# Performance work log

Measured on AMD Instinct MI355X. Metric: run time of the kernel, lower is better.

Reference implementation:

```python
import jax, jax.numpy as jnp
import numpy as np

LN_EPS = 1e-6          # flax nn.LayerNorm default
ATTN_EPS = 1e-9        # numerical_stabilizer default


def ln_points(x, scale, bias):
    """flax LayerNorm(reduction_axes=-2): stats over points axis, affine over feature axis."""
    mu = jnp.mean(x, axis=-2, keepdims=True)
    var = jnp.mean(jnp.square(x), axis=-2, keepdims=True) - jnp.square(mu)
    return (x - mu) * jax.lax.rsqrt(var + LN_EPS) * scale + bias


def self_attention_layer(x, wq_i, bq_i, wk_i, bk_i, wv_i, bv_i, wo_i, bo_i, ls_i, lb_i):
    # 1x1 convs == pointwise linears
    q = x @ wq_i + bq_i                                  # [B,N,C]
    k = x @ wk_i + bk_i
    v = x @ wv_i + bv_i
    attn = jnp.einsum('bmc,bnc->bmn', q, k)              # [B,M,N]
    attn = jax.nn.softmax(attn, axis=-1)
    # extra offset-attention renorm: divide by column sums (axis=1)
    attn = attn / (ATTN_EPS + jnp.sum(attn, axis=1, keepdims=True))
    # einsum '...MN,...NC->...NC' reduces M: scales v by column sums
    col = jnp.sum(attn, axis=1)                          # [B,N]
    out = col[..., None] * v                             # [B,N,C]
    out = out @ wo_i + bo_i
    out = jax.nn.relu(ln_points(out, ls_i, lb_i))
    return out + x


def setup_inputs() -> dict:
    key = jax.random.key(0)
    ks = jax.random.split(key, 16)
    B, N, IN, C, F, L = 2, 4096, 3, 256, 1024, 4
    s_in = 1.0 / np.sqrt(IN)
    s_c = 1.0 / np.sqrt(C)
    s_f = 1.0 / np.sqrt(L * C)
    return {
        'inputs': jax.random.normal(ks[0], (B, N, IN), jnp.float32),
        'w0': jax.random.normal(ks[1], (IN, C), jnp.float32) * s_in,
        'b0': jnp.zeros((C,), jnp.float32),
        'ln0_s': jnp.ones((C,), jnp.float32),
        'ln0_b': jnp.zeros((C,), jnp.float32),
        'w1': jax.random.normal(ks[2], (C, C), jnp.float32) * s_c,
        'b1': jnp.zeros((C,), jnp.float32),
        'ln1_s': jnp.ones((C,), jnp.float32),
        'ln1_b': jnp.zeros((C,), jnp.float32),
        'wq': jax.random.normal(ks[3], (L, C, C), jnp.float32) * s_c,
        'bq': jnp.zeros((L, C), jnp.float32),
        'wk': jax.random.normal(ks[4], (L, C, C), jnp.float32) * s_c,
        'bk': jnp.zeros((L, C), jnp.float32),
        'wv': jax.random.normal(ks[5], (L, C, C), jnp.float32) * s_c,
        'bv': jnp.zeros((L, C), jnp.float32),
        'wo': jax.random.normal(ks[6], (L, C, C), jnp.float32) * s_c,
        'bo': jnp.zeros((L, C), jnp.float32),
        'attn_ln_s': jnp.ones((L, C), jnp.float32),
        'attn_ln_b': jnp.zeros((L, C), jnp.float32),
        'wf': jax.random.normal(ks[7], (L * C, F), jnp.float32) * s_f,
        'bf': jnp.zeros((F,), jnp.float32),
    }


def reference(inputs, w0, b0, ln0_s, ln0_b, w1, b1, ln1_s, ln1_b,
              wq, bq, wk, bk, wv, bv, wo, bo, attn_ln_s, attn_ln_b, wf, bf):
    # pre-conv stack
    out = ln_points(inputs @ w0 + b0, ln0_s, ln0_b)
    out = ln_points(out @ w1 + b1, ln1_s, ln1_b)
    # attention stack (4 structurally identical layers, concatenated)
    attn_outs = []
    for i in range(wq.shape[0]):
        out = self_attention_layer(out, wq[i], bq[i], wk[i], bk[i],
                                   wv[i], bv[i], wo[i], bo[i],
                                   attn_ln_s[i], attn_ln_b[i])
        attn_outs.append(out)
    out = jnp.concatenate(attn_outs, axis=-1)            # [B,N,4C]
    out = out @ wf + bf                                  # [B,N,F]
    return out
```

## Files before the change

### kernel.cpp

```cpp
#include <hip/hip_runtime.h>

#define BB 2
#define NN 4096
#define CC 256
#define FF 1024
#define NLAYER 4
#define RR (BB*NN)
#define SPL 16
#define QKLD (3*CC)
#define NEG_BIG (-1e30f)

typedef _Float16 h16;
typedef __attribute__((ext_vector_type(8))) _Float16 half8;
typedef __attribute__((ext_vector_type(4))) float f32x4;
typedef __attribute__((ext_vector_type(16))) float f32x16;

__device__ __forceinline__ void gload16(const h16* g, h16* l) {
    __builtin_amdgcn_global_load_lds((const __attribute__((address_space(1))) void*)g,
                                     (__attribute__((address_space(3))) void*)l, 16, 0, 0);
}

template<int ROWS>
__device__ __forceinline__ void stage_rows(const h16* __restrict__ src, int ld,
    int row0, int c0, h16* lds, int tid)
{
    int w = tid >> 6;
    #pragma unroll
    for (int t = 0; t < ROWS/32; ++t) {
        int slot = t*256 + tid;
        int row = slot >> 3;
        int pp  = slot & 7;
        int piece = pp ^ (row & 7);
        gload16(src + (size_t)(row0 + row)*ld + c0 + piece*8,
                lds + (t*256 + w*64)*8);
    }
}

__device__ __forceinline__ half8 frag_ld(const h16* lds, int row, int pl) {
    return *(const half8*)(lds + row*64 + ((pl ^ (row & 7))*8));
}

__global__ __launch_bounds__(256) void pct_wtrans(const float* __restrict__ W,
    h16* __restrict__ WT, int K, int N, int dstride)
{
    __shared__ h16 t[32][33];
    const float* Wl = W + (size_t)blockIdx.z*K*N;
    h16* WTl = WT + (size_t)blockIdx.z*dstride;
    int k0 = blockIdx.x*32, n0 = blockIdx.y*32;
    int tx = threadIdx.x & 31, ty = threadIdx.x >> 5;
    #pragma unroll
    for (int i = ty; i < 32; i += 8)
        t[i][tx] = (h16)Wl[(size_t)(k0+i)*N + n0 + tx];
    __syncthreads();
    #pragma unroll
    for (int i = ty; i < 32; i += 8)
        WTl[(size_t)(n0+i)*K + k0 + tx] = t[tx][i];
}

__global__ __launch_bounds__(256) void pct_bias3(const float* __restrict__ bq,
    const float* __restrict__ bk, const float* __restrict__ bv, float* __restrict__ o)
{
    int l = blockIdx.x, c = threadIdx.x;
    o[l*QKLD + c]        = bq[l*CC + c];
    o[l*QKLD + CC + c]   = bk[l*CC + c];
    o[l*QKLD + 2*CC + c] = bv[l*CC + c];
}

__global__ __launch_bounds__(256) void pct_embed(const float* __restrict__ inp,
    const float* __restrict__ w0, const float* __restrict__ b0, h16* __restrict__ out)
{
    int r = blockIdx.x, c = threadIdx.x;
    float a0 = inp[r*3+0], a1 = inp[r*3+1], a2 = inp[r*3+2];
    out[(size_t)r*CC + c] = (h16)(b0[c] + a0*w0[c] + a1*w0[CC+c] + a2*w0[2*CC+c]);
}

__global__ __launch_bounds__(256) void pct_colstat(const h16* __restrict__ x, int ldx,
    float* __restrict__ sums)
{
    __shared__ float red[2][8][256];
    int b = blockIdx.x, blk = blockIdx.y;
    int rt = threadIdx.x >> 5;
    int cg = (threadIdx.x & 31) * 8;
    const h16* p = x + ((size_t)b*NN + (size_t)blk*64 + rt)*ldx + cg;
    float s1[8] = {0,0,0,0,0,0,0,0}, s2[8] = {0,0,0,0,0,0,0,0};
    #pragma unroll
    for (int i = 0; i < 8; ++i) {
        half8 v = *(const half8*)(p + (size_t)i*8*ldx);
        #pragma unroll
        for (int j = 0; j < 8; ++j) { float f = (float)v[j]; s1[j] += f; s2[j] += f*f; }
    }
    #pragma unroll
    for (int j = 0; j < 8; ++j) { red[0][rt][cg+j] = s1[j]; red[1][rt][cg+j] = s2[j]; }
    __syncthreads();
    int c = threadIdx.x;
    float t1 = 0.f, t2 = 0.f;
    #pragma unroll
    for (int r = 0; r < 8; ++r) { t1 += red[0][r][c]; t2 += red[1][r][c]; }
    atomicAdd(&sums[(b*CC + c)*2 + 0], t1);
    atomicAdd(&sums[(b*CC + c)*2 + 1], t2);
}

__global__ __launch_bounds__(256) void pct_lnapply(const h16* __restrict__ x, int ldx,
    const float* __restrict__ sums, const float* __restrict__ scale, const float* __restrict__ bias,
    const h16* __restrict__ res, int ldr, h16* __restrict__ out, int ldo,
    int do_relu)
{
    int r = blockIdx.x*8 + (threadIdx.x >> 5);
    int cg = (threadIdx.x & 31) * 8;
    int b = r / NN;
    half8 xv = *(const half8*)(x + (size_t)r*ldx + cg);
    half8 rv;
    if (res) rv = *(const half8*)(res + (size_t)r*ldr + cg);
    half8 ov;
    #pragma unroll
    for (int j = 0; j < 8; ++j) {
        int c = cg + j;
        float s1 = sums[(b*CC + c)*2], s2 = sums[(b*CC + c)*2 + 1];
        float mu  = s1 * (1.f/NN);
        float var = s2 * (1.f/NN) - mu*mu;
        float rstd = rsqrtf(var + 1e-6f);
        float y = ((float)xv[j] - mu) * rstd * scale[c] + bias[c];
        if (do_relu) y = fmaxf(y, 0.f);
        if (res) y += (float)rv[j];
        ov[j] = (h16)y;
    }
    *(half8*)(out + (size_t)r*ldo + cg) = ov;
}

template<int BN, bool OUT_F32>
__global__ __launch_bounds__(256) void pct_gemm_f16(
    const h16* __restrict__ A, int lda,
    const h16* __restrict__ WT, const float* __restrict__ bias,
    void* __restrict__ outp, int ldo, int K, const float* __restrict__ rowS)
{
    constexpr int BJ = BN/2;
    constexpr int NF = BJ/16;
    __shared__ __align__(16) h16 Asm[128*64];
    __shared__ __align__(16) h16 Bsm[BN*64];
    const int tid = threadIdx.x;
    const int lane = tid & 63, w = tid >> 6;
    const int ln = lane & 15, lq = lane >> 4;
    const int wr = w >> 1, wc = w & 1;
    const int m0 = blockIdx.x*128, n0 = blockIdx.y*BN;
    f32x4 acc[4][NF];
    #pragma unroll
    for (int i = 0; i < 4; ++i)
        #pragma unroll
        for (int j = 0; j < NF; ++j) acc[i][j] = (f32x4){0.f,0.f,0.f,0.f};
    for (int k0 = 0; k0 < K; k0 += 64) {
        stage_rows<128>(A, lda, m0, k0, Asm, tid);
        stage_rows<BN>(WT, K, n0, k0, Bsm, tid);
        __syncthreads();
        #pragma unroll
        for (int kk = 0; kk < 2; ++kk) {
            half8 af[4], bfr[NF];
            #pragma unroll
            for (int i = 0; i < 4; ++i) af[i] = frag_ld(Asm, wr*64 + i*16 + ln, kk*4 + lq);
            #pragma unroll
            for (int j = 0; j < NF; ++j) bfr[j] = frag_ld(Bsm, wc*BJ + j*16 + ln, kk*4 + lq);
            #pragma unroll
            for (int i = 0; i < 4; ++i)
                #pragma unroll
                for (int j = 0; j < NF; ++j)
                    acc[i][j] = __builtin_amdgcn_mfma_f32_16x16x32_f16(af[i], bfr[j], acc[i][j], 0, 0, 0);
        }
        __syncthreads();
    }
    #pragma unroll
    for (int j = 0; j < NF; ++j) {
        int col = n0 + wc*BJ + j*16 + ln;
        float bv = bias[col];
        #pragma unroll
        for (int i = 0; i < 4; ++i) {
            #pragma unroll
            for (int r = 0; r < 4; ++r) {
                int row = m0 + wr*64 + i*16 + lq*4 + r;
                float sc = 1.f;
                if (rowS) { float s = rowS[row]; sc = s / (1e-9f + s); }
                float v = acc[i][j][r] * sc + bv;
                if (OUT_F32) ((float*)outp)[(size_t)row*ldo + col] = v;
                else ((h16*)outp)[(size_t)row*ldo + col] = (h16)v;
            }
        }
    }
}

__global__ __launch_bounds__(256) void attn_rowstats(const h16* __restrict__ QKV,
    float2* __restrict__ part)
{
    __shared__ __align__(16) h16 Ks[2][128*64];
    const int b = blockIdx.x, mt = blockIdx.y, sp = blockIdx.z;
    const int tid = threadIdx.x;
    const int lane = tid & 63, w = tid >> 6;
    const int ln2 = lane & 31, h = lane >> 5;
    const h16* qb = QKV + (size_t)b*NN*QKLD;
    const h16* kb = qb + CC;
    const int m0 = mt*128;
    const h16* qrow = qb + (size_t)(m0 + w*32 + ln2)*QKLD + h*8;
    half8 qreg[16];
    #pragma unroll
    for (int i = 0; i < 16; ++i) qreg[i] = *(const half8*)(qrow + i*16);

    const int nbeg = sp*(NN/SPL);
    const int NT = (NN/SPL)/128;
    float rm = NEG_BIG, rs = 0.f;

    stage_rows<128>(kb, QKLD, nbeg, 0, Ks[0], tid);
    int id = 0;
    for (int t = 0; t < NT; ++t) {
        f32x16 acc[4];
        #pragma unroll
        for (int j = 0; j < 4; ++j) acc[j] = (f32x16)(0.f);
        #pragma unroll
        for (int c = 0; c < 4; ++c, ++id) {
            __syncthreads();
            if (id + 1 < NT*4)
                stage_rows<128>(kb, QKLD, nbeg + ((id+1) >> 2)*128, ((id+1) & 3)*64,
                                Ks[(id+1) & 1], tid);
            const h16* buf = Ks[id & 1];
            #pragma unroll
            for (int kk = 0; kk < 4; ++kk) {
                half8 bq = qreg[c*4 + kk];
                #pragma unroll
                for (int j = 0; j < 4; ++j) {
                    half8 af = frag_ld(buf, j*32 + ln2, kk*2 + h);
                    acc[j] = __builtin_amdgcn_mfma_f32_32x32x16_f16(af, bq, acc[j], 0, 0, 0);
                }
            }
        }
        float tm = NEG_BIG;
        #pragma unroll
        for (int j = 0; j < 4; ++j)
            #pragma unroll
            for (int g = 0; g < 16; g += 2)
                tm = fmaxf(tm, fmaxf(acc[j][g], acc[j][g+1]));
        if (tm > rm) { rs *= __expf(rm - tm); rm = tm; }
        float s = 0.f;
        #pragma unroll
        for (int j = 0; j < 4; ++j)
            #pragma unroll
            for (int g = 0; g < 16; ++g)
                s += __expf(acc[j][g] - rm);
        rs += s;
    }
    float mo = __shfl_xor(rm, 32, 64);
    float so = __shfl_xor(rs, 32, 64);
    float mn = fmaxf(rm, mo);
    float sm = rs*__expf(rm - mn) + so*__expf(mo - mn);
    if (lane < 32) {
        int m = m0 + w*32 + ln2;
        part[((size_t)b*NN + m)*SPL + sp] = make_float2(mn, sm);
    }
}

__global__ __launch_bounds__(256) void pct_rowcomb(const float2* __restrict__ part,
    float2* __restrict__ rstat)
{
    int idx = blockIdx.x*256 + threadIdx.x;
    const float2* p = part + (size_t)idx*SPL;
    float m = NEG_BIG;
    #pragma unroll
    for (int s = 0; s < SPL; ++s) m = fmaxf(m, p[s].x);
    float sum = 0.f;
    #pragma unroll
    for (int s = 0; s < SPL; ++s) sum += p[s].y * __expf(p[s].x - m);
    rstat[idx] = make_float2(m, 1.0f / sum);
}

__global__ __launch_bounds__(256) void attn_colsums(const h16* __restrict__ QKV,
    const float2* __restrict__ rstat, float* __restrict__ S)
{
    __shared__ __align__(16) h16 Qs[2][128*64];
    const int b = blockIdx.x, nt = blockIdx.y, sp = blockIdx.z;
    const int tid = threadIdx.x;
    const int lane = tid & 63, w = tid >> 6;
    const int ln2 = lane & 31, h = lane >> 5;
    const h16* qb = QKV + (size_t)b*NN*QKLD;
    const h16* kb = qb + CC;
    const float2* rst = rstat + (size_t)b*NN;
    const int n0 = nt*128;
    const h16* krow = kb + (size_t)(n0 + w*32 + ln2)*QKLD + h*8;
    half8 kreg[16];
    #pragma unroll
    for (int i = 0; i < 16; ++i) kreg[i] = *(const half8*)(krow + i*16);

    const int mbeg = sp*(NN/SPL);
    const int NT = (NN/SPL)/128;
    float cs = 0.f;

    stage_rows<128>(qb, QKLD, mbeg, 0, Qs[0], tid);
    int id = 0;
    for (int t = 0; t < NT; ++t) {
        f32x16 acc[4];
        #pragma unroll
        for (int j = 0; j < 4; ++j) acc[j] = (f32x16)(0.f);
        #pragma unroll
        for (int c = 0; c < 4; ++c, ++id) {
            __syncthreads();
            if (id + 1 < NT*4)
                stage_rows<128>(qb, QKLD, mbeg + ((id+1) >> 2)*128, ((id+1) & 3)*64,
                                Qs[(id+1) & 1], tid);
            const h16* buf = Qs[id & 1];
            #pragma unroll
            for (int kk = 0; kk < 4; ++kk) {
                half8 bk = kreg[c*4 + kk];
                #pragma unroll
                for (int j = 0; j < 4; ++j) {
                    half8 af = frag_ld(buf, j*32 + ln2, kk*2 + h);
                    acc[j] = __builtin_amdgcn_mfma_f32_32x32x16_f16(af, bk, acc[j], 0, 0, 0);
                }
            }
        }
        int mt0 = mbeg + t*128;
        #pragma unroll
        for (int j = 0; j < 4; ++j) {
            #pragma unroll
            for (int g = 0; g < 16; ++g) {
                int m = mt0 + j*32 + (g & 3) + 8*(g >> 2) + 4*h;
                float2 st = rst[m];
                cs += __expf(acc[j][g] - st.x) * st.y;
            }
        }
    }
    cs += __shfl_xor(cs, 32, 64);
    if (lane < 32) {
        int n = n0 + w*32 + ln2;
        atomicAdd(&S[(size_t)b*NN + n], cs);
    }
}

extern "C" void kernel_launch(void* const* d_in, const int* in_sizes, int n_in,
                              void* d_out, int out_size, void* d_ws, size_t ws_size,
                              hipStream_t stream)
{
    const float* inp  = (const float*)d_in[0];
    const float* w0   = (const float*)d_in[1];
    const float* b0   = (const float*)d_in[2];
    const float* ln0s = (const float*)d_in[3];
    const float* ln0b = (const float*)d_in[4];
    const float* w1   = (const float*)d_in[5];
    const float* b1   = (const float*)d_in[6];
    const float* ln1s = (const float*)d_in[7];
    const float* ln1b = (const float*)d_in[8];
    const float* wq   = (const float*)d_in[9];
    const float* bq   = (const float*)d_in[10];
    const float* wk   = (const float*)d_in[11];
    const float* bk   = (const float*)d_in[12];
    const float* wv   = (const float*)d_in[13];
    const float* bv   = (const float*)d_in[14];
    const float* wo   = (const float*)d_in[15];
    const float* bo   = (const float*)d_in[16];
    const float* alns = (const float*)d_in[17];
    const float* alnb = (const float*)d_in[18];
    const float* wf   = (const float*)d_in[19];
    const float* bfb  = (const float*)d_in[20];
    float* out = (float*)d_out;

    char* p = (char*)d_ws;
    auto alloc = [&](size_t bytes) { char* r = p; p += (bytes + 255) & ~255ULL; return r; };
    h16* t0    = (h16*)alloc((size_t)RR*CC*2);
    h16* t1    = (h16*)alloc((size_t)RR*CC*2);
    h16* t2    = (h16*)alloc((size_t)RR*CC*2);
    h16* x1    = (h16*)alloc((size_t)RR*CC*2);
    h16* qkv   = (h16*)alloc((size_t)RR*QKLD*2);
    h16* oh    = (h16*)alloc((size_t)RR*CC*2);
    h16* xcat  = (h16*)alloc((size_t)RR*FF*2);
    h16* w1T   = (h16*)alloc((size_t)CC*CC*2);
    h16* wqkvT = (h16*)alloc((size_t)NLAYER*QKLD*CC*2);
    h16* woT   = (h16*)alloc((size_t)NLAYER*CC*CC*2);
    h16* wfT   = (h16*)alloc((size_t)FF*FF*2);
    float* bqkv  = (float*)alloc((size_t)NLAYER*QKLD*4);
    float2* part  = (float2*)alloc((size_t)RR*SPL*8);
    float2* rstat = (float2*)alloc((size_t)RR*8);
    float* Ssum  = (float*)alloc((size_t)NLAYER*RR*4);
    float* lns   = (float*)alloc((size_t)6*BB*CC*2*4);

    dim3 blk(256);

    hipMemsetAsync(Ssum, 0, (size_t)((char*)(lns + 6*BB*CC*2) - (char*)Ssum), stream);

    pct_wtrans<<<dim3(CC/32, CC/32, 1), blk, 0, stream>>>(w1, w1T, CC, CC, CC*CC);
    pct_wtrans<<<dim3(CC/32, CC/32, NLAYER), blk, 0, stream>>>(wq, wqkvT,            CC, CC, QKLD*CC);
    pct_wtrans<<<dim3(CC/32, CC/32, NLAYER), blk, 0, stream>>>(wk, wqkvT + CC*CC,    CC, CC, QKLD*CC);
    pct_wtrans<<<dim3(CC/32, CC/32, NLAYER), blk, 0, stream>>>(wv, wqkvT + 2*CC*CC,  CC, CC, QKLD*CC);
    pct_wtrans<<<dim3(CC/32, CC/32, NLAYER), blk, 0, stream>>>(wo, woT, CC, CC, CC*CC);
    pct_wtrans<<<dim3(FF/32, FF/32, 1), blk, 0, stream>>>(wf, wfT, FF, FF, FF*FF);
    pct_bias3<<<NLAYER, blk, 0, stream>>>(bq, bk, bv, bqkv);

    pct_embed<<<RR, blk, 0, stream>>>(inp, w0, b0, t0);
    pct_colstat<<<dim3(BB,64), blk, 0, stream>>>(t0, CC, lns + 0*BB*CC*2);
    pct_lnapply<<<RR/8, blk, 0, stream>>>(t0, CC, lns + 0*BB*CC*2, ln0s, ln0b, nullptr, 0, t1, CC, 0);
    pct_gemm_f16<64,false><<<dim3(RR/128, CC/64), blk, 0, stream>>>(t1, CC, w1T, b1, t2, CC, CC, nullptr);
    pct_colstat<<<dim3(BB,64), blk, 0, stream>>>(t2, CC, lns + 1*BB*CC*2);
    pct_lnapply<<<RR/8, blk, 0, stream>>>(t2, CC, lns + 1*BB*CC*2, ln1s, ln1b, nullptr, 0, x1, CC, 0);

    const h16* xin = x1; int ldx = CC;
    for (int i = 0; i < NLAYER; ++i) {
        pct_gemm_f16<64,false><<<dim3(RR/128, QKLD/64), blk, 0, stream>>>(
            xin, ldx, wqkvT + (size_t)i*QKLD*CC, bqkv + i*QKLD, qkv, QKLD, CC, nullptr);

        attn_rowstats<<<dim3(BB, NN/128, SPL), blk, 0, stream>>>(qkv, part);
        pct_rowcomb<<<RR/256, blk, 0, stream>>>(part, rstat);
        attn_colsums<<<dim3(BB, NN/128, SPL), blk, 0, stream>>>(qkv, rstat, Ssum + (size_t)i*RR);

        pct_gemm_f16<64,false><<<dim3(RR/128, CC/64), blk, 0, stream>>>(
            qkv + 2*CC, QKLD, woT + (size_t)i*CC*CC, bo + i*CC, oh, CC, CC, Ssum + (size_t)i*RR);

        pct_colstat<<<dim3(BB,64), blk, 0, stream>>>(oh, CC, lns + (2+i)*BB*CC*2);
        pct_lnapply<<<RR/8, blk, 0, stream>>>(oh, CC, lns + (2+i)*BB*CC*2, alns + i*CC, alnb + i*CC,
                                              xin, ldx, xcat + i*CC, FF, 1);
        xin = xcat + i*CC; ldx = FF;
    }

    pct_gemm_f16<128,true><<<dim3(RR/128, FF/128), blk, 0, stream>>>(xcat, FF, wfT, bfb, out, FF, FF, nullptr);
}
```

Baseline: 560.5 us.

## Fuse LayerNorm column statistics into GEMM epilogues and use exp2 softmax

Removes the separate column-statistics kernels. The sums and sums of squares are now accumulated in the GEMM epilogue, and in the embed kernel, then reduced with shuffles, shared memory and atomics. Q weights and bias are prescaled by log2(e) so the attention kernels can use exp2f instead of __expf, and the three QKV weight transposes are merged into one launch. This saves several launches and full re-reads of activations. In exchange the GEMM gets extra epilogue work, and the stats are taken from fp32 values rather than the rounded fp16 outputs.

```diff
diff --git a/kernel.cpp b/kernel.cpp
--- a/kernel.cpp
+++ b/kernel.cpp
@@ -9,6 +9,7 @@
 #define SPL 16
 #define QKLD (3*CC)
 #define NEG_BIG (-1e30f)
+#define LOG2E 1.44269504f
 
 typedef _Float16 h16;
 typedef __attribute__((ext_vector_type(8))) _Float16 half8;
@@ -41,7 +42,7 @@
 }
 
 __global__ __launch_bounds__(256) void pct_wtrans(const float* __restrict__ W,
-    h16* __restrict__ WT, int K, int N, int dstride)
+    h16* __restrict__ WT, int K, int N, int dstride, float scale)
 {
     __shared__ h16 t[32][33];
     const float* Wl = W + (size_t)blockIdx.z*K*N;
@@ -50,54 +51,62 @@
     int tx = threadIdx.x & 31, ty = threadIdx.x >> 5;
     #pragma unroll
     for (int i = ty; i < 32; i += 8)
-        t[i][tx] = (h16)Wl[(size_t)(k0+i)*N + n0 + tx];
+        t[i][tx] = (h16)(Wl[(size_t)(k0+i)*N + n0 + tx] * scale);
     __syncthreads();
     #pragma unroll
     for (int i = ty; i < 32; i += 8)
         WTl[(size_t)(n0+i)*K + k0 + tx] = t[tx][i];
 }
 
+__global__ __launch_bounds__(256) void pct_wtrans_qkv(const float* __restrict__ wq,
+    const float* __restrict__ wk, const float* __restrict__ wv, h16* __restrict__ WT)
+{
+    __shared__ h16 t[32][33];
+    int z = blockIdx.z;
+    int which = z >> 2, layer = z & 3;
+    const float* Wl = (which == 0 ? wq : which == 1 ? wk : wv) + (size_t)layer*CC*CC;
+    h16* WTl = WT + (size_t)layer*QKLD*CC + (size_t)which*CC*CC;
+    float scale = (which == 0) ? LOG2E : 1.0f;
+    int k0 = blockIdx.x*32, n0 = blockIdx.y*32;
+    int tx = threadIdx.x & 31, ty = threadIdx.x >> 5;
+    #pragma unroll
+    for (int i = ty; i < 32; i += 8)
+        t[i][tx] = (h16)(Wl[(size_t)(k0+i)*CC + n0 + tx] * scale);
+    __syncthreads();
+    #pragma unroll
+    for (int i = ty; i < 32; i += 8)
+        WTl[(size_t)(n0+i)*CC + k0 + tx] = t[tx][i];
+}
+
 __global__ __launch_bounds__(256) void pct_bias3(const float* __restrict__ bq,
     const float* __restrict__ bk, const float* __restrict__ bv, float* __restrict__ o)
 {
     int l = blockIdx.x, c = threadIdx.x;
-    o[l*QKLD + c]        = bq[l*CC + c];
+    o[l*QKLD + c]        = bq[l*CC + c] * LOG2E;
     o[l*QKLD + CC + c]   = bk[l*CC + c];
     o[l*QKLD + 2*CC + c] = bv[l*CC + c];
 }
 
 __global__ __launch_bounds__(256) void pct_embed(const float* __restrict__ inp,
-    const float* __restrict__ w0, const float* __restrict__ b0, h16* __restrict__ out)
-{
-    int r = blockIdx.x, c = threadIdx.x;
-    float a0 = inp[r*3+0], a1 = inp[r*3+1], a2 = inp[r*3+2];
-    out[(size_t)r*CC + c] = (h16)(b0[c] + a0*w0[c] + a1*w0[CC+c] + a2*w0[2*CC+c]);
-}
-
-__global__ __launch_bounds__(256) void pct_colstat(const h16* __restrict__ x, int ldx,
-    float* __restrict__ sums)
-{
-    __shared__ float red[2][8][256];
-    int b = blockIdx.x, blk = blockIdx.y;
-    int rt = threadIdx.x >> 5;
-    int cg = (threadIdx.x & 31) * 8;
-    const h16* p = x + ((size_t)b*NN + (size_t)blk*64 + rt)*ldx + cg;
-    float s1[8] = {0,0,0,0,0,0,0,0}, s2[8] = {0,0,0,0,0,0,0,0};
-    #pragma unroll
-    for (int i = 0; i < 8; ++i) {
-        half8 v = *(const half8*)(p + (size_t)i*8*ldx);
-        #pragma unroll
-        for (int j = 0; j < 8; ++j) { float f = (float)v[j]; s1[j] += f; s2[j] += f*f; }
-    }
-    #pragma unroll
-    for (int j = 0; j < 8; ++j) { red[0][rt][cg+j] = s1[j]; red[1][rt][cg+j] = s2[j]; }
-    __syncthreads();
+    const float* __restrict__ w0, const float* __restrict__ b0,
+    h16* __restrict__ out, float* __restrict__ sums)
+{
     int c = threadIdx.x;
-    float t1 = 0.f, t2 = 0.f;
-    #pragma unroll
-    for (int r = 0; r < 8; ++r) { t1 += red[0][r][c]; t2 += red[1][r][c]; }
-    atomicAdd(&sums[(b*CC + c)*2 + 0], t1);
-    atomicAdd(&sums[(b*CC + c)*2 + 1], t2);
+    int r0 = blockIdx.x * 64;
+    float wa = w0[c], wb = w0[CC+c], wcv = w0[2*CC+c], bb = b0[c];
+    float s1 = 0.f, s2 = 0.f;
+    #pragma unroll 4
+    for (int i = 0; i < 64; ++i) {
+        int r = r0 + i;
+        float y = bb + inp[r*3+0]*wa + inp[r*3+1]*wb + inp[r*3+2]*wcv;
+        h16 hy = (h16)y;
+        out[(size_t)r*CC + c] = hy;
+        float yf = (float)hy;
+        s1 += yf; s2 += yf*yf;
+    }
+    int b = r0 >> 12;
+    atomicAdd(&sums[((size_t)b*CC + c)*2 + 0], s1);
+    atomicAdd(&sums[((size_t)b*CC + c)*2 + 1], s2);
 }
 
 __global__ __launch_bounds__(256) void pct_lnapply(const h16* __restrict__ x, int ldx,
@@ -127,11 +136,12 @@
     *(half8*)(out + (size_t)r*ldo + cg) = ov;
 }
 
-template<int BN, bool OUT_F32>
+template<int BN, bool OUT_F32, bool CSTAT>
 __global__ __launch_bounds__(256) void pct_gemm_f16(
     const h16* __restrict__ A, int lda,
     const h16* __restrict__ WT, const float* __restrict__ bias,
-    void* __restrict__ outp, int ldo, int K, const float* __restrict__ rowS)
+    void* __restrict__ outp, int ldo, int K, const float* __restrict__ rowS,
+    float* __restrict__ csums)
 {
     constexpr int BJ = BN/2;
     constexpr int NF = BJ/16;
@@ -166,10 +176,12 @@
         }
         __syncthreads();
     }
+    float cs1[NF], cs2[NF];
     #pragma unroll
     for (int j = 0; j < NF; ++j) {
         int col = n0 + wc*BJ + j*16 + ln;
         float bv = bias[col];
+        float s1 = 0.f, s2 = 0.f;
         #pragma unroll
         for (int i = 0; i < 4; ++i) {
             #pragma unroll
@@ -180,7 +192,30 @@
                 float v = acc[i][j][r] * sc + bv;
                 if (OUT_F32) ((float*)outp)[(size_t)row*ldo + col] = v;
                 else ((h16*)outp)[(size_t)row*ldo + col] = (h16)v;
+                if (CSTAT) { s1 += v; s2 += v*v; }
             }
+        }
+        cs1[j] = s1; cs2[j] = s2;
+    }
+    if constexpr (CSTAT) {
+        __shared__ float cred[2][2][BJ][2];
+        #pragma unroll
+        for (int j = 0; j < NF; ++j) {
+            float s1 = cs1[j], s2 = cs2[j];
+            s1 += __shfl_down(s1, 16); s1 += __shfl_down(s1, 32);
+            s2 += __shfl_down(s2, 16); s2 += __shfl_down(s2, 32);
+            if (lane < 16) {
+                cred[wr][wc][j*16 + lane][0] = s1;
+                cred[wr][wc][j*16 + lane][1] = s2;
+            }
+        }
+        __syncthreads();
+        if (tid < 2*BN) {
+            int c = tid >> 1, st = tid & 1;
+            int wcc = c >> 5, ci = c & 31;
+            float v = cred[0][wcc][ci][st] + cred[1][wcc][ci][st];
+            int b = m0 >> 12;
+            atomicAdd(&csums[((size_t)b*CC + n0 + c)*2 + st], v);
         }
     }
 }
@@ -234,19 +269,19 @@
             #pragma unroll
             for (int g = 0; g < 16; g += 2)
                 tm = fmaxf(tm, fmaxf(acc[j][g], acc[j][g+1]));
-        if (tm > rm) { rs *= __expf(rm - tm); rm = tm; }
+        if (tm > rm) { rs *= exp2f(rm - tm); rm = tm; }
         float s = 0.f;
         #pragma unroll
         for (int j = 0; j < 4; ++j)
             #pragma unroll
             for (int g = 0; g < 16; ++g)
-                s += __expf(acc[j][g] - rm);
+                s += exp2f(acc[j][g] - rm);
         rs += s;
     }
     float mo = __shfl_xor(rm, 32, 64);
     float so = __shfl_xor(rs, 32, 64);
     float mn = fmaxf(rm, mo);
-    float sm = rs*__expf(rm - mn) + so*__expf(mo - mn);
+    float sm = rs*exp2f(rm - mn) + so*exp2f(mo - mn);
     if (lane < 32) {
         int m = m0 + w*32 + ln2;
         part[((size_t)b*NN + m)*SPL + sp] = make_float2(mn, sm);
@@ -263,7 +298,7 @@
     for (int s = 0; s < SPL; ++s) m = fmaxf(m, p[s].x);
     float sum = 0.f;
     #pragma unroll
-    for (int s = 0; s < SPL; ++s) sum += p[s].y * __expf(p[s].x - m);
+    for (int s = 0; s < SPL; ++s) sum += p[s].y * exp2f(p[s].x - m);
     rstat[idx] = make_float2(m, 1.0f / sum);
 }
 
@@ -318,7 +353,7 @@
             for (int g = 0; g < 16; ++g) {
                 int m = mt0 + j*32 + (g & 3) + 8*(g >> 2) + 4*h;
                 float2 st = rst[m];
-                cs += __expf(acc[j][g] - st.x) * st.y;
+                cs += exp2f(acc[j][g] - st.x) * st.y;
             }
         }
     }
@@ -379,38 +414,36 @@
 
     hipMemsetAsync(Ssum, 0, (size_t)((char*)(lns + 6*BB*CC*2) - (char*)Ssum), stream);
 
-    pct_wtrans<<<dim3(CC/32, CC/32, 1), blk, 0, stream>>>(w1, w1T, CC, CC, CC*CC);
-    pct_wtrans<<<dim3(CC/32, CC/32, NLAYER), blk, 0, stream>>>(wq, wqkvT,            CC, CC, QKLD*CC);
-    pct_wtrans<<<dim3(CC/32, CC/32, NLAYER), blk, 0, stream>>>(wk, wqkvT + CC*CC,    CC, CC, QKLD*CC);
-    pct_wtrans<<<dim3(CC/32, CC/32, NLAYER), blk, 0, stream>>>(wv, wqkvT + 2*CC*CC,  CC, CC, QKLD*CC);
-    pct_wtrans<<<dim3(CC/32, CC/32, NLAYER), blk, 0, stream>>>(wo, woT, CC, CC, CC*CC);
-    pct_wtrans<<<dim3(FF/32, FF/32, 1), blk, 0, stream>>>(wf, wfT, FF, FF, FF*FF);
+    pct_wtrans<<<dim3(CC/32, CC/32, 1), blk, 0, stream>>>(w1, w1T, CC, CC, CC*CC, 1.f);
+    pct_wtrans_qkv<<<dim3(CC/32, CC/32, 3*NLAYER), blk, 0, stream>>>(wq, wk, wv, wqkvT);
+    pct_wtrans<<<dim3(CC/32, CC/32, NLAYER), blk, 0, stream>>>(wo, woT, CC, CC, CC*CC, 1.f);
+    pct_wtrans<<<dim3(FF/32, FF/32, 1), blk, 0, stream>>>(wf, wfT, FF, FF, FF*FF, 1.f);
     pct_bias3<<<NLAYER, blk, 0, stream>>>(bq, bk, bv, bqkv);
 
-    pct_embed<<<RR, blk, 0, stream>>>(inp, w0, b0, t0);
-    pct_colstat<<<dim3(BB,64), blk, 0, stream>>>(t0, CC, lns + 0*BB*CC*2);
+    pct_embed<<<RR/64, blk, 0, stream>>>(inp, w0, b0, t0, lns + 0*BB*CC*2);
     pct_lnapply<<<RR/8, blk, 0, stream>>>(t0, CC, lns + 0*BB*CC*2, ln0s, ln0b, nullptr, 0, t1, CC, 0);
-    pct_gemm_f16<64,false><<<dim3(RR/128, CC/64), blk, 0, stream>>>(t1, CC, w1T, b1, t2, CC, CC, nullptr);
-    pct_colstat<<<dim3(BB,64), blk, 0, stream>>>(t2, CC, lns + 1*BB*CC*2);
+    pct_gemm_f16<64,false,true><<<dim3(RR/128, CC/64), blk, 0, stream>>>(
+        t1, CC, w1T, b1, t2, CC, CC, nullptr, lns + 1*BB*CC*2);
     pct_lnapply<<<RR/8, blk, 0, stream>>>(t2, CC, lns + 1*BB*CC*2, ln1s, ln1b, nullptr, 0, x1, CC, 0);
 
     const h16* xin = x1; int ldx = CC;
     for (int i = 0; i < NLAYER; ++i) {
-        pct_gemm_f16<64,false><<<dim3(RR/128, QKLD/64), blk, 0, stream>>>(
-            xin, ldx, wqkvT + (size_t)i*QKLD*CC, bqkv + i*QKLD, qkv, QKLD, CC, nullptr);
+        pct_gemm_f16<64,false,false><<<dim3(RR/128, QKLD/64), blk, 0, stream>>>(
+            xin, ldx, wqkvT + (size_t)i*QKLD*CC, bqkv + i*QKLD, qkv, QKLD, CC, nullptr, nullptr);
 
         attn_rowstats<<<dim3(BB, NN/128, SPL), blk, 0, stream>>>(qkv, part);
         pct_rowcomb<<<RR/256, blk, 0, stream>>>(part, rstat);
         attn_colsums<<<dim3(BB, NN/128, SPL), blk, 0, stream>>>(qkv, rstat, Ssum + (size_t)i*RR);
 
-        pct_gemm_f16<64,false><<<dim3(RR/128, CC/64), blk, 0, stream>>>(
-            qkv + 2*CC, QKLD, woT + (size_t)i*CC*CC, bo + i*CC, oh, CC, CC, Ssum + (size_t)i*RR);
-
-        pct_colstat<<<dim3(BB,64), blk, 0, stream>>>(oh, CC, lns + (2+i)*BB*CC*2);
+        pct_gemm_f16<64,false,true><<<dim3(RR/128, CC/64), blk, 0, stream>>>(
+            qkv + 2*CC, QKLD, woT + (size_t)i*CC*CC, bo + i*CC, oh, CC, CC,
+            Ssum + (size_t)i*RR, lns + (2+i)*BB*CC*2);
+
         pct_lnapply<<<RR/8, blk, 0, stream>>>(oh, CC, lns + (2+i)*BB*CC*2, alns + i*CC, alnb + i*CC,
                                               xin, ldx, xcat + i*CC, FF, 1);
         xin = xcat + i*CC; ldx = FF;
     }
 
-    pct_gemm_f16<128,true><<<dim3(RR/128, FF/128), blk, 0, stream>>>(xcat, FF, wfT, bfb, out, FF, FF, nullptr);
-}
+    pct_gemm_f16<128,true,false><<<dim3(RR/128, FF/128), blk, 0, stream>>>(
+        xcat, FF, wfT, bfb, out, FF, FF, nullptr, nullptr);
+}
```

New measurement: 554.8 us. No clear change (-1.0%).
